# Kernel tuning notes

Hardware: AMD Instinct MI355X
Metric: run time of the kernel (lower is better)

## Reference

```python
import jax, jax.numpy as jnp
import numpy as np

B, T, D, H, L, P = 256, 96, 64, 256, 5, 14
H2 = 2 * H   # decoder hidden
O = D        # output_size must equal input_size (decoder feeds its own output back)


def setup_inputs() -> dict:
    key = jax.random.key(0)
    ks = iter(jax.random.split(key, 32))
    s = 0.08  # weight scale to keep gates out of saturation
    rn = lambda shape, sc=s: jax.random.normal(next(ks), shape, jnp.float32) * sc
    return dict(
        x=rn((B, T, D), 1.0),
        # encoder: bidirectional, layer 0 input=D, layers 1..4 input=2H
        enc_Wih0=rn((2, 4 * H, D)), enc_Whh0=rn((2, 4 * H, H)),
        enc_bih0=rn((2, 4 * H)), enc_bhh0=rn((2, 4 * H)),
        enc_Wih=rn((L - 1, 2, 4 * H, 2 * H)), enc_Whh=rn((L - 1, 2, 4 * H, H)),
        enc_bih=rn((L - 1, 2, 4 * H)), enc_bhh=rn((L - 1, 2, 4 * H)),
        # decoder: unidirectional, hidden=2H, layer 0 input=D, layers 1..4 input=2H
        dec_Wih0=rn((4 * H2, D)), dec_Whh0=rn((4 * H2, H2)),
        dec_bih0=rn((4 * H2,)), dec_bhh0=rn((4 * H2,)),
        dec_Wih=rn((L - 1, 4 * H2, H2)), dec_Whh=rn((L - 1, 4 * H2, H2)),
        dec_bih=rn((L - 1, 4 * H2)), dec_bhh=rn((L - 1, 4 * H2)),
        fc_W=rn((O, H2)), fc_b=rn((O,)),
    )


def _lstm_cell(x, h, c, Wih, Whh, bih, bhh):
    # PyTorch gate order: i, f, g, o
    g = x @ Wih.T + h @ Whh.T + (bih + bhh)
    i, f, gg, o = jnp.split(g, 4, axis=-1)
    c = jax.nn.sigmoid(f) * c + jax.nn.sigmoid(i) * jnp.tanh(gg)
    h = jax.nn.sigmoid(o) * jnp.tanh(c)
    return h, c


def _scan_dir(xs, Wih, Whh, bih, bhh, reverse):
    # xs: (T, B, Din); returns per-step hidden (T,B,Hn) + final (h, c)
    Bn, Hn = xs.shape[1], Whh.shape[-1]
    z = jnp.zeros((Bn, Hn), xs.dtype)

    def step(carry, xt):
        h, c = carry
        h, c = _lstm_cell(xt, h, c, Wih, Whh, bih, bhh)
        return (h, c), h

    (hT, cT), hs = jax.lax.scan(step, (z, z), xs, reverse=reverse)
    return hs, hT, cT


def _forward(x, enc_Wih0, enc_Whh0, enc_bih0, enc_bhh0,
             enc_Wih, enc_Whh, enc_bih, enc_bhh,
             dec_Wih0, dec_Whh0, dec_bih0, dec_bhh0,
             dec_Wih, dec_Whh, dec_bih, dec_bhh, fc_W, fc_b):
    xs = jnp.swapaxes(x, 0, 1)  # (T, B, D)
    inp = xs
    h_fin, c_fin = [], []
    for l in range(L):
        if l == 0:
            Wih, Whh, bih, bhh = enc_Wih0, enc_Whh0, enc_bih0, enc_bhh0
        else:
            Wih, Whh, bih, bhh = enc_Wih[l - 1], enc_Whh[l - 1], enc_bih[l - 1], enc_bhh[l - 1]
        hs_f, hTf, cTf = _scan_dir(inp, Wih[0], Whh[0], bih[0], bhh[0], False)
        hs_b, hTb, cTb = _scan_dir(inp, Wih[1], Whh[1], bih[1], bhh[1], True)
        inp = jnp.concatenate([hs_f, hs_b], axis=-1)  # (T, B, 2H)
        # matches h_n.view(L,2,B,H).transpose(1,2).view(L,B,2H): per layer [fwd, bwd]
        h_fin.append(jnp.concatenate([hTf, hTb], axis=-1))
        c_fin.append(jnp.concatenate([cTf, cTb], axis=-1))
    h0 = jnp.stack(h_fin)  # (L, B, 2H)
    c0 = jnp.stack(c_fin)

    dec_params = [(dec_Wih0, dec_Whh0, dec_bih0, dec_bhh0)] + \
                 [(dec_Wih[l], dec_Whh[l], dec_bih[l], dec_bhh[l]) for l in range(L - 1)]

    def dec_step(carry, _):
        h, c, xt = carry
        z = xt
        nh, nc = [], []
        for l, (Wih, Whh, bih, bhh) in enumerate(dec_params):
            hl, cl = _lstm_cell(z, h[l], c[l], Wih, Whh, bih, bhh)
            z = hl
            nh.append(hl); nc.append(cl)
        out = z @ fc_W.T + fc_b  # (B, O); fed back as next decoder input
        return (jnp.stack(nh), jnp.stack(nc), out), out

    _, outs = jax.lax.scan(dec_step, (h0, c0, x[:, -1, :]), None, length=P)
    return jnp.swapaxes(outs, 0, 1)  # (B, P, O)


def reference(x, enc_Wih0, enc_Whh0, enc_bih0, enc_bhh0,
              enc_Wih, enc_Whh, enc_bih, enc_bhh,
              dec_Wih0, dec_Whh0, dec_bih0, dec_bhh0,
              dec_Wih, dec_Whh, dec_bih, dec_bhh, fc_W, fc_b):
    return _forward(x, enc_Wih0, enc_Whh0, enc_bih0, enc_bhh0,
                    enc_Wih, enc_Whh, enc_bih, enc_bhh,
                    dec_Wih0, dec_Whh0, dec_bih0, dec_bhh0,
                    dec_Wih, dec_Whh, dec_bih, dec_bhh, fc_W, fc_b)
```

## Files before the change

### kernel.cpp

```cpp
#include <hip/hip_runtime.h>

typedef _Float16 f16;
using half8 = __attribute__((ext_vector_type(8))) _Float16;
using half4 = __attribute__((ext_vector_type(4))) _Float16;
using f32x4 = __attribute__((ext_vector_type(4))) float;

#define DEV __device__ __forceinline__
#define LD8(p) (*(const half8*)(const void*)(p))

DEV f32x4 mfma16(half8 a, half8 b, f32x4 c) {
  return __builtin_amdgcn_mfma_f32_16x16x32_f16(a, b, c, 0, 0, 0);
}
DEV float sigf(float x) { return 1.f / (1.f + __expf(-x)); }
DEV float tanhf2(float x) { float e = __expf(2.f * x); return 1.f - 2.f / (e + 1.f); }

static const size_t OFF_WIH0   = 0;
static const size_t OFF_WIH14  = 262144;
static const size_t OFF_WHH    = 8650752;
static const size_t OFF_WDEC0  = 13893632;
static const size_t OFF_WDEC14 = 16252928;
static const size_t OFF_WFC    = 33030144;
static const size_t OFF_X16    = 33095680;
static const size_t OFF_SEQA   = 36241408;
static const size_t OFF_SEQB   = 61407232;
static const size_t OFF_XG     = 86573056;
static const size_t OFF_HBUF   = 187236352;
static const size_t OFF_FLAGS  = 187760640;
static const size_t OFF_DHDB   = 188284928;
static const size_t OFF_DCST   = 190906368;
static const size_t OFF_ZFC    = 193527808;

__global__ __launch_bounds__(256) void prep(
    const float* __restrict__ x,
    const float* __restrict__ eWih0, const float* __restrict__ eWhh0,
    const float* __restrict__ eWih,  const float* __restrict__ eWhh,
    const float* __restrict__ dWih0, const float* __restrict__ dWhh0,
    const float* __restrict__ dWih,  const float* __restrict__ dWhh,
    const float* __restrict__ fcW,   char* __restrict__ ws)
{
  f16* wih0   = (f16*)(ws + OFF_WIH0);
  f16* wih14  = (f16*)(ws + OFF_WIH14);
  f16* whhf   = (f16*)(ws + OFF_WHH);
  f16* wdec0  = (f16*)(ws + OFF_WDEC0);
  f16* wdec14 = (f16*)(ws + OFF_WDEC14);
  f16* wfc    = (f16*)(ws + OFF_WFC);
  f16* x16    = (f16*)(ws + OFF_X16);
  f16* zfc    = (f16*)(ws + OFF_ZFC);
  int* flags  = (int*)(ws + OFF_FLAGS);
  const size_t total = 18137152;
  for (size_t i = (size_t)blockIdx.x * blockDim.x + threadIdx.x; i < total;
       i += (size_t)gridDim.x * blockDim.x) {
    size_t j = i;
    if (j < 131072) { wih0[j] = (f16)eWih0[j]; continue; }
    j -= 131072;
    if (j < 4194304) { wih14[j] = (f16)eWih[j]; continue; }
    j -= 4194304;
    if (j < 2621440) {
      size_t l = j >> 19, i2 = j & 524287;
      int d   = (int)(i2 >> 18);
      int uh  = (int)((i2 >> 17) & 1);
      int w   = (int)((i2 >> 14) & 7);
      int g   = (int)((i2 >> 12) & 3);
      int kc  = (int)((i2 >> 9) & 7);
      int lnv = (int)((i2 >> 3) & 63);
      int e   = (int)(i2 & 7);
      int unit = uh * 128 + w * 16 + (lnv & 15);
      int k = kc * 32 + (lnv >> 4) * 8 + e;
      int row = g * 256 + unit;
      float v = (l == 0) ? eWhh0[((size_t)d * 1024 + row) * 256 + k]
                         : eWhh[((((l - 1) * 2 + (size_t)d) * 1024) + row) * 256 + k];
      whhf[j] = (f16)v;
      continue;
    }
    j -= 2621440;
    if (j < 1179648) {
      size_t r = j / 576, c = j % 576;
      wdec0[j] = (f16)((c < 64) ? dWih0[r * 64 + c] : dWhh0[r * 512 + (c - 64)]);
      continue;
    }
    j -= 1179648;
    if (j < 8388608) {
      size_t l = j >> 21, rem = j & 2097151;
      size_t r = rem >> 10, c = rem & 1023;
      wdec14[j] = (f16)((c < 512) ? dWih[(l * 2048 + r) * 512 + c]
                                  : dWhh[(l * 2048 + r) * 512 + (c - 512)]);
      continue;
    }
    j -= 8388608;
    if (j < 32768) { wfc[j] = (f16)fcW[j]; continue; }
    j -= 32768;
    if (j < 1572864) {
      size_t t = j >> 14, rem = j & 16383;
      size_t b = rem >> 6, d = rem & 63;
      x16[j] = (f16)x[(b * 96 + t) * 64 + d];
      continue;
    }
    j -= 1572864;
    if (j < 16384) {
      size_t b = j >> 6, d = j & 63;
      zfc[b * 512 + d] = (f16)x[(b * 96 + 95) * 64 + d];
      continue;
    }
    j -= 16384;
    flags[j] = 0;
  }
}

__global__ __launch_bounds__(256) void gemm_xg(
    const f16* __restrict__ A, int K, const f16* __restrict__ W,
    const float* __restrict__ bih, const float* __restrict__ bhh,
    f16* __restrict__ xg)
{
  __shared__ __align__(16) f16 As[128 * 32];
  __shared__ __align__(16) f16 Ws[128 * 32];
  const int dir = blockIdx.y >> 3;
  const int cb  = (blockIdx.y & 7) * 128;
  const int rb  = blockIdx.x * 128;
  const int tid = threadIdx.x;
  const int wv = tid >> 6, ln = tid & 63;
  const int wr = wv >> 1, wc = wv & 1;
  const f16* Wd = W + (size_t)dir * 1024 * K;

  f32x4 acc[4][4];
#pragma unroll
  for (int m = 0; m < 4; m++)
#pragma unroll
    for (int n = 0; n < 4; n++) acc[m][n] = (f32x4){0.f, 0.f, 0.f, 0.f};

  const int sr = tid >> 1;
  const int sk = (tid & 1) * 16;
  const int nk = K >> 5;
  for (int kt = 0; kt < nk; ++kt) {
    half8 va0 = LD8(&A[(size_t)(rb + sr) * K + kt * 32 + sk]);
    half8 va1 = LD8(&A[(size_t)(rb + sr) * K + kt * 32 + sk + 8]);
    half8 vw0 = LD8(&Wd[(size_t)(cb + sr) * K + kt * 32 + sk]);
    half8 vw1 = LD8(&Wd[(size_t)(cb + sr) * K + kt * 32 + sk + 8]);
    *(half8*)&As[sr * 32 + sk] = va0;
    *(half8*)&As[sr * 32 + sk + 8] = va1;
    *(half8*)&Ws[sr * 32 + sk] = vw0;
    *(half8*)&Ws[sr * 32 + sk + 8] = vw1;
    __syncthreads();
    half8 af[4], bf[4];
#pragma unroll
    for (int m = 0; m < 4; m++)
      af[m] = LD8(&As[(wr * 64 + m * 16 + (ln & 15)) * 32 + (ln >> 4) * 8]);
#pragma unroll
    for (int n = 0; n < 4; n++)
      bf[n] = LD8(&Ws[(wc * 64 + n * 16 + (ln & 15)) * 32 + (ln >> 4) * 8]);
#pragma unroll
    for (int m = 0; m < 4; m++)
#pragma unroll
      for (int n = 0; n < 4; n++) acc[m][n] = mfma16(af[m], bf[n], acc[m][n]);
    __syncthreads();
  }
#pragma unroll
  for (int n = 0; n < 4; n++) {
    const int col = cb + wc * 64 + n * 16 + (ln & 15);
    const float bsum = bih[dir * 1024 + col] + bhh[dir * 1024 + col];
    const int c16 = (cb + wc * 64 + n * 16) >> 4;
#pragma unroll
    for (int m = 0; m < 4; m++) {
      const int r16 = (rb + wr * 64 + m * 16) >> 4;
      half4 h;
#pragma unroll
      for (int r = 0; r < 4; r++) h[r] = (f16)(acc[m][n][r] + bsum);
      *(half4*)&xg[(((size_t)dir * 1536 + r16) * 64 + c16) * 256 + ln * 4] = h;
    }
  }
}

__global__ __launch_bounds__(512) __attribute__((amdgpu_waves_per_eu(2, 2)))
void enc_layer(
    const f16* __restrict__ xg, const f16* __restrict__ whhf,
    f16* __restrict__ hbuf, int* __restrict__ flags,
    f16* __restrict__ seqo, f16* __restrict__ hfin, float* __restrict__ cfin,
    int layer)
{
  const int bb = blockIdx.x;
  const int d = blockIdx.y >> 1, uh = blockIdx.y & 1;
  const int tid = threadIdx.x;
  const int wv = tid >> 6, ln = tid & 63;
  const int lc = ln & 15, lk = ln >> 4;

  __shared__ __align__(16) char hl[2][4096];

  half8 wfr[32];
  const f16* wbase = whhf + (((size_t)(d * 2 + uh) * 8 + wv) * 16384);
#pragma unroll
  for (int g = 0; g < 4; g++) {
#pragma unroll
    for (int jj = 0; jj < 4; jj++) {
      wfr[g * 8 + jj]     = LD8(&wbase[(size_t)(g * 8 + uh * 4 + jj) * 512 + ln * 8]);
      wfr[g * 8 + 4 + jj] = LD8(&wbase[(size_t)(g * 8 + (1 - uh) * 4 + jj) * 512 + ln * 8]);
    }
  }
#pragma unroll
  for (int i = 0; i < 32; i++) asm volatile("" : "+v"(wfr[i]));

  f16* hown = hbuf + ((size_t)((bb * 2 + d) * 2 + uh)) * 4096;
  const f16* hpart = hbuf + ((size_t)((bb * 2 + d) * 2 + (uh ^ 1))) * 4096;
  int* myflag = &flags[(bb * 2 + d) * 2 + uh];
  int* pflag  = &flags[(bb * 2 + d) * 2 + (uh ^ 1)];
  const int base = layer * 96;
  const int rowbase = bb * 16;
  const int unit_local = wv * 16 + lc;
  const int cu = uh * 128 + unit_local;
  const int erow = tid >> 5, ec8 = tid & 31;
  const int eba = (erow * 256 + ec8 * 8) ^ ((erow & 7) << 4);

  f32x4 cst = (f32x4){0.f, 0.f, 0.f, 0.f};
  f32x4 ownp[4];
#pragma unroll
  for (int g = 0; g < 4; g++) ownp[g] = (f32x4){0.f, 0.f, 0.f, 0.f};

  for (int t = 0; t < 96; ++t) {
    const int tt = d ? 95 - t : t;
    const int par = (t - 1) & 1, par2 = t & 1;
    const int r16 = tt * 16 + bb;
    half4 xv[4];
#pragma unroll
    for (int g = 0; g < 4; g++)
      xv[g] = *(const half4*)&xg[(((size_t)d * 1536 + r16) * 64 +
                                  (g * 16 + uh * 8 + wv)) * 256 + ln * 4];
    f32x4 acc[4];
#pragma unroll
    for (int g = 0; g < 4; g++) {
#pragma unroll
      for (int r = 0; r < 4; r++) acc[g][r] = ownp[g][r] + (float)xv[g][r];
    }
    if (t > 0) {
      unsigned spin = 0;
      while (__hip_atomic_load(pflag, __ATOMIC_RELAXED,
                               __HIP_MEMORY_SCOPE_AGENT) < base + t) {
        if (++spin > 65536u) break;
      }
      asm volatile("" ::: "memory");
      unsigned long long q[4][2];
#pragma unroll
      for (int j = 0; j < 4; j++) {
        const f16* p = &hpart[par * 2048 + lc * 128 + j * 32 + lk * 8];
        q[j][0] = __hip_atomic_load((const unsigned long long*)p,
                                    __ATOMIC_RELAXED, __HIP_MEMORY_SCOPE_AGENT);
        q[j][1] = __hip_atomic_load((const unsigned long long*)(p + 4),
                                    __ATOMIC_RELAXED, __HIP_MEMORY_SCOPE_AGENT);
      }
#pragma unroll
      for (int j = 0; j < 4; j++) {
        union { unsigned long long uq[2]; half8 h; } u;
        u.uq[0] = q[j][0]; u.uq[1] = q[j][1];
#pragma unroll
        for (int g = 0; g < 4; g++)
          acc[g] = mfma16(u.h, wfr[g * 8 + 4 + j], acc[g]);
      }
    }
    f16 hv[4];
#pragma unroll
    for (int r = 0; r < 4; r++) {
      float gi = sigf(acc[0][r]);
      float gf = sigf(acc[1][r]);
      float gg = tanhf2(acc[2][r]);
      float go = sigf(acc[3][r]);
      float cn = gf * cst[r] + gi * gg;
      cst[r] = cn;
      hv[r] = (f16)(go * tanhf2(cn));
    }
#pragma unroll
    for (int r = 0; r < 4; r++) {
      int row = lk * 4 + r;
      int ba = (row * 256 + unit_local * 2) ^ ((row & 7) << 4);
      *(f16*)&hl[par2][ba] = hv[r];
    }
    __syncthreads();
    unsigned long long v = *(const unsigned long long*)&hl[par2][eba];
    __hip_atomic_store((unsigned long long*)&hown[par2 * 2048 + erow * 128 + ec8 * 4],
                       v, __ATOMIC_RELAXED, __HIP_MEMORY_SCOPE_AGENT);
    asm volatile("s_waitcnt vmcnt(0)" ::: "memory");
    __syncthreads();
    if (tid == 0)
      __hip_atomic_store(myflag, base + t + 1, __ATOMIC_RELAXED,
                         __HIP_MEMORY_SCOPE_AGENT);
    *(unsigned long long*)&seqo[(size_t)tt * 131072 +
        (size_t)(rowbase + erow) * 512 + d * 256 + uh * 128 + ec8 * 4] = v;
    if (t == 95) {
      *(unsigned long long*)&hfin[(size_t)(rowbase + erow) * 512 +
                                  d * 256 + uh * 128 + ec8 * 4] = v;
#pragma unroll
      for (int r = 0; r < 4; r++)
        cfin[(size_t)(rowbase + lk * 4 + r) * 512 + d * 256 + cu] = cst[r];
    } else {
      half8 ao[4];
#pragma unroll
      for (int j = 0; j < 4; j++) {
        int ba = (lc * 256 + j * 64 + lk * 16) ^ ((lc & 7) << 4);
        ao[j] = *(const half8*)&hl[par2][ba];
      }
#pragma unroll
      for (int g = 0; g < 4; g++) {
        f32x4 s = (f32x4){0.f, 0.f, 0.f, 0.f};
#pragma unroll
        for (int j = 0; j < 4; j++) s = mfma16(ao[j], wfr[g * 8 + j], s);
        ownp[g] = s;
      }
    }
  }
}

__global__ __launch_bounds__(128) void dec_step(
    const f16* __restrict__ A0, int K0, const f16* __restrict__ A1,
    const f16* __restrict__ W, int Kt,
    const float* __restrict__ bih, const float* __restrict__ bhh,
    float* __restrict__ cst, f16* __restrict__ h1)
{
  const int u0 = blockIdx.y * 32;
  const int rb = blockIdx.x * 64;
  const int wv = threadIdx.x >> 6, ln = threadIdx.x & 63;
  const int lc = ln & 15, lk = ln >> 4;
  const int cu = u0 + wv * 16 + lc;
  f32x4 acc[4][4];
#pragma unroll
  for (int g = 0; g < 4; g++) {
    float b = bih[g * 512 + cu] + bhh[g * 512 + cu];
#pragma unroll
    for (int rr = 0; rr < 4; rr++) acc[rr][g] = (f32x4){b, b, b, b};
  }
  const int K0c = K0 >> 5, Ktc = Kt >> 5;
  for (int kc = 0; kc < Ktc; kc++) {
    const f16* Ap; int ko;
    if (kc < K0c) { Ap = A0; ko = kc * 32; }
    else          { Ap = A1; ko = (kc - K0c) * 32; }
    half8 b[4];
#pragma unroll
    for (int g = 0; g < 4; g++)
      b[g] = LD8(&W[(size_t)(g * 512 + cu) * Kt + kc * 32 + lk * 8]);
#pragma unroll
    for (int rr = 0; rr < 4; rr++) {
      half8 a = LD8(&Ap[(size_t)(rb + rr * 16 + lc) * 512 + ko + lk * 8]);
#pragma unroll
      for (int g = 0; g < 4; g++) acc[rr][g] = mfma16(a, b[g], acc[rr][g]);
    }
  }
#pragma unroll
  for (int rr = 0; rr < 4; rr++) {
#pragma unroll
    for (int r = 0; r < 4; r++) {
      const int row = rb + rr * 16 + lk * 4 + r;
      float gi = sigf(acc[rr][0][r]);
      float gf = sigf(acc[rr][1][r]);
      float gg = tanhf2(acc[rr][2][r]);
      float go = sigf(acc[rr][3][r]);
      float cp = cst[(size_t)row * 512 + cu];
      float cn = gf * cp + gi * gg;
      cst[(size_t)row * 512 + cu] = cn;
      h1[(size_t)row * 512 + cu] = (f16)(go * tanhf2(cn));
    }
  }
}

__global__ __launch_bounds__(64) void fc_kernel(
    const f16* __restrict__ hin, const f16* __restrict__ Wf,
    const float* __restrict__ bf, float* __restrict__ out,
    f16* __restrict__ zfc, int s)
{
  const int rb = blockIdx.x * 16;
  const int ln = threadIdx.x;
  f32x4 acc[4];
#pragma unroll
  for (int n = 0; n < 4; n++) acc[n] = (f32x4){0.f, 0.f, 0.f, 0.f};
#pragma unroll
  for (int kc = 0; kc < 16; kc++) {
    half8 a = LD8(&hin[(size_t)(rb + (ln & 15)) * 512 + kc * 32 + (ln >> 4) * 8]);
#pragma unroll
    for (int n = 0; n < 4; n++) {
      half8 b = LD8(&Wf[(size_t)(n * 16 + (ln & 15)) * 512 + kc * 32 + (ln >> 4) * 8]);
      acc[n] = mfma16(a, b, acc[n]);
    }
  }
#pragma unroll
  for (int n = 0; n < 4; n++) {
    const int col = n * 16 + (ln & 15);
    const float bb = bf[col];
#pragma unroll
    for (int r = 0; r < 4; r++) {
      const int row = rb + (ln >> 4) * 4 + r;
      float v = acc[n][r] + bb;
      out[(size_t)row * 896 + s * 64 + col] = v;
      zfc[(size_t)row * 512 + col] = (f16)v;
    }
  }
}

extern "C" void kernel_launch(void* const* d_in, const int* in_sizes, int n_in,
                              void* d_out, int out_size, void* d_ws, size_t ws_size,
                              hipStream_t stream) {
  char* ws = (char*)d_ws;
  const float* x     = (const float*)d_in[0];
  const float* eWih0 = (const float*)d_in[1];
  const float* eWhh0 = (const float*)d_in[2];
  const float* ebih0 = (const float*)d_in[3];
  const float* ebhh0 = (const float*)d_in[4];
  const float* eWih  = (const float*)d_in[5];
  const float* eWhh  = (const float*)d_in[6];
  const float* ebih  = (const float*)d_in[7];
  const float* ebhh  = (const float*)d_in[8];
  const float* dWih0 = (const float*)d_in[9];
  const float* dWhh0 = (const float*)d_in[10];
  const float* dbih0 = (const float*)d_in[11];
  const float* dbhh0 = (const float*)d_in[12];
  const float* dWih  = (const float*)d_in[13];
  const float* dWhh  = (const float*)d_in[14];
  const float* dbih  = (const float*)d_in[15];
  const float* dbhh  = (const float*)d_in[16];
  const float* fcW   = (const float*)d_in[17];
  const float* fcb   = (const float*)d_in[18];

  f16* xg    = (f16*)(ws + OFF_XG);
  f16* hbuf  = (f16*)(ws + OFF_HBUF);
  int* flags = (int*)(ws + OFF_FLAGS);
  f16* dhdb  = (f16*)(ws + OFF_DHDB);
  float* dcst = (float*)(ws + OFF_DCST);
  f16* zfc   = (f16*)(ws + OFF_ZFC);
  f16* seqA  = (f16*)(ws + OFF_SEQA);
  f16* seqB  = (f16*)(ws + OFF_SEQB);

  prep<<<dim3(2048), dim3(256), 0, stream>>>(x, eWih0, eWhh0, eWih, eWhh,
                                             dWih0, dWhh0, dWih, dWhh, fcW, ws);

  for (int l = 0; l < 5; ++l) {
    const f16* Ain = (l == 0) ? (f16*)(ws + OFF_X16) : ((l & 1) ? seqA : seqB);
    const int K = (l == 0) ? 64 : 512;
    const f16* Wih = (l == 0) ? (f16*)(ws + OFF_WIH0)
                              : (f16*)(ws + OFF_WIH14) + (size_t)(l - 1) * 2 * 1024 * 512;
    const float* bi = (l == 0) ? ebih0 : ebih + (size_t)(l - 1) * 2048;
    const float* bh = (l == 0) ? ebhh0 : ebhh + (size_t)(l - 1) * 2048;
    gemm_xg<<<dim3(192, 16), dim3(256), 0, stream>>>(Ain, K, Wih, bi, bh, xg);

    const f16* whhf_l = (f16*)(ws + OFF_WHH) + (size_t)l * 524288;
    f16* so = (l & 1) ? seqB : seqA;
    enc_layer<<<dim3(16, 4), dim3(512), 0, stream>>>(
        xg, whhf_l, hbuf, flags, so,
        dhdb + (size_t)l * 131072, dcst + (size_t)l * 131072, l);
  }

  for (int s = 0; s < 14; ++s) {
    const int p = s & 1;
    for (int l = 0; l < 5; ++l) {
      dec_step<<<dim3(4, 16), dim3(128), 0, stream>>>(
          (l == 0) ? zfc : dhdb + (size_t)(p ^ 1) * 655360 + (size_t)(l - 1) * 131072,
          (l == 0) ? 64 : 512,
          dhdb + (size_t)p * 655360 + (size_t)l * 131072,
          (l == 0) ? (f16*)(ws + OFF_WDEC0)
                   : (f16*)(ws + OFF_WDEC14) + (size_t)(l - 1) * 2048 * 1024,
          (l == 0) ? 576 : 1024,
          (l == 0) ? dbih0 : dbih + (size_t)(l - 1) * 2048,
          (l == 0) ? dbhh0 : dbhh + (size_t)(l - 1) * 2048,
          dcst + (size_t)l * 131072,
          dhdb + (size_t)(p ^ 1) * 655360 + (size_t)l * 131072);
    }
    fc_kernel<<<dim3(16), dim3(64), 0, stream>>>(
        dhdb + (size_t)(p ^ 1) * 655360 + 4 * 131072, (f16*)(ws + OFF_WFC), fcb,
        (float*)d_out, zfc, s);
  }
}
```

Measured before the change: 4.279 ms.

## Split encoder recurrence across 8 unit-slices per direction with LDS-resident weights

Reworks the encoder recurrent kernel so each (batch block, direction) is served by 8 small 128-thread workgroups, each owning 32 hidden units, instead of 2 large 512-thread workgroups. Recurrent weights now sit in LDS rather than registers. Each step waits on flags from all 8 peers and reads the full hidden state from global memory, dropping the own-half precomputation trick. The aim is more parallel workgroups and less register pressure, at the cost of more cross-workgroup synchronisation and global traffic per timestep. The prep kernel's weight permutation and element count change to match the new layout.

```diff
diff --git a/kernel.cpp b/kernel.cpp
--- a/kernel.cpp
+++ b/kernel.cpp
@@ -47,7 +47,7 @@
   f16* x16    = (f16*)(ws + OFF_X16);
   f16* zfc    = (f16*)(ws + OFF_ZFC);
   int* flags  = (int*)(ws + OFF_FLAGS);
-  const size_t total = 18137152;
+  const size_t total = 18137344;
   for (size_t i = (size_t)blockIdx.x * blockDim.x + threadIdx.x; i < total;
        i += (size_t)gridDim.x * blockDim.x) {
     size_t j = i;
@@ -58,13 +58,13 @@
     if (j < 2621440) {
       size_t l = j >> 19, i2 = j & 524287;
       int d   = (int)(i2 >> 18);
-      int uh  = (int)((i2 >> 17) & 1);
-      int w   = (int)((i2 >> 14) & 7);
+      int uo  = (int)((i2 >> 15) & 7);
+      int tile= (int)((i2 >> 14) & 1);
       int g   = (int)((i2 >> 12) & 3);
       int kc  = (int)((i2 >> 9) & 7);
       int lnv = (int)((i2 >> 3) & 63);
       int e   = (int)(i2 & 7);
-      int unit = uh * 128 + w * 16 + (lnv & 15);
+      int unit = uo * 32 + tile * 16 + (lnv & 15);
       int k = kc * 32 + (lnv >> 4) * 8 + e;
       int row = g * 256 + unit;
       float v = (l == 0) ? eWhh0[((size_t)d * 1024 + row) * 256 + k]
@@ -169,49 +169,37 @@
   }
 }
 
-__global__ __launch_bounds__(512) __attribute__((amdgpu_waves_per_eu(2, 2)))
-void enc_layer(
+__global__ __launch_bounds__(128) void enc_layer(
     const f16* __restrict__ xg, const f16* __restrict__ whhf,
     f16* __restrict__ hbuf, int* __restrict__ flags,
     f16* __restrict__ seqo, f16* __restrict__ hfin, float* __restrict__ cfin,
     int layer)
 {
   const int bb = blockIdx.x;
-  const int d = blockIdx.y >> 1, uh = blockIdx.y & 1;
+  const int d = blockIdx.y >> 3, uo = blockIdx.y & 7;
   const int tid = threadIdx.x;
   const int wv = tid >> 6, ln = tid & 63;
   const int lc = ln & 15, lk = ln >> 4;
 
-  __shared__ __align__(16) char hl[2][4096];
-
-  half8 wfr[32];
-  const f16* wbase = whhf + (((size_t)(d * 2 + uh) * 8 + wv) * 16384);
-#pragma unroll
-  for (int g = 0; g < 4; g++) {
-#pragma unroll
-    for (int jj = 0; jj < 4; jj++) {
-      wfr[g * 8 + jj]     = LD8(&wbase[(size_t)(g * 8 + uh * 4 + jj) * 512 + ln * 8]);
-      wfr[g * 8 + 4 + jj] = LD8(&wbase[(size_t)(g * 8 + (1 - uh) * 4 + jj) * 512 + ln * 8]);
-    }
-  }
-#pragma unroll
-  for (int i = 0; i < 32; i++) asm volatile("" : "+v"(wfr[i]));
-
-  f16* hown = hbuf + ((size_t)((bb * 2 + d) * 2 + uh)) * 4096;
-  const f16* hpart = hbuf + ((size_t)((bb * 2 + d) * 2 + (uh ^ 1))) * 4096;
-  int* myflag = &flags[(bb * 2 + d) * 2 + uh];
-  int* pflag  = &flags[(bb * 2 + d) * 2 + (uh ^ 1)];
+  __shared__ __align__(16) f16 wL[32768];
+  __shared__ __align__(16) f16 hB[16 * 36];
+
+  const f16* wsrc = whhf + (size_t)(d * 8 + uo) * 32768;
+#pragma unroll 4
+  for (int i = 0; i < 32; i++)
+    *(half8*)&wL[(i * 128 + tid) * 8] = LD8(&wsrc[(size_t)(i * 128 + tid) * 8]);
+  __syncthreads();
+
+  int* gflags = &flags[(bb * 2 + d) * 8];
+  int* myflag = &gflags[uo];
+  const f16* hgrp = hbuf + (size_t)(bb * 2 + d) * 8192;
+  f16* hown = hbuf + (size_t)((bb * 2 + d) * 8 + uo) * 1024;
   const int base = layer * 96;
   const int rowbase = bb * 16;
-  const int unit_local = wv * 16 + lc;
-  const int cu = uh * 128 + unit_local;
-  const int erow = tid >> 5, ec8 = tid & 31;
-  const int eba = (erow * 256 + ec8 * 8) ^ ((erow & 7) << 4);
+  const int cu = uo * 32 + wv * 16 + lc;
+  const int erow = tid >> 3, eu8 = tid & 7;
 
   f32x4 cst = (f32x4){0.f, 0.f, 0.f, 0.f};
-  f32x4 ownp[4];
-#pragma unroll
-  for (int g = 0; g < 4; g++) ownp[g] = (f32x4){0.f, 0.f, 0.f, 0.f};
 
   for (int t = 0; t < 96; ++t) {
     const int tt = d ? 95 - t : t;
@@ -221,36 +209,48 @@
 #pragma unroll
     for (int g = 0; g < 4; g++)
       xv[g] = *(const half4*)&xg[(((size_t)d * 1536 + r16) * 64 +
-                                  (g * 16 + uh * 8 + wv)) * 256 + ln * 4];
-    f32x4 acc[4];
-#pragma unroll
-    for (int g = 0; g < 4; g++) {
-#pragma unroll
-      for (int r = 0; r < 4; r++) acc[g][r] = ownp[g][r] + (float)xv[g][r];
-    }
+                                  (g * 16 + uo * 2 + wv)) * 256 + ln * 4];
+    unsigned long long q[8][2];
     if (t > 0) {
-      unsigned spin = 0;
-      while (__hip_atomic_load(pflag, __ATOMIC_RELAXED,
-                               __HIP_MEMORY_SCOPE_AGENT) < base + t) {
-        if (++spin > 65536u) break;
+      if (tid == 0) {
+        unsigned spin = 0;
+        for (;;) {
+          int mn = 0x7fffffff;
+#pragma unroll
+          for (int p = 0; p < 8; p++) {
+            int f = __hip_atomic_load(&gflags[p], __ATOMIC_RELAXED,
+                                      __HIP_MEMORY_SCOPE_AGENT);
+            mn = (f < mn) ? f : mn;
+          }
+          if (mn >= base + t || ++spin > 100000u) break;
+          __builtin_amdgcn_s_sleep(1);
+        }
       }
-      asm volatile("" ::: "memory");
-      unsigned long long q[4][2];
-#pragma unroll
-      for (int j = 0; j < 4; j++) {
-        const f16* p = &hpart[par * 2048 + lc * 128 + j * 32 + lk * 8];
+      __syncthreads();
+#pragma unroll
+      for (int j = 0; j < 8; j++) {
+        const f16* p = hgrp + (size_t)(j * 2 + par) * 512 + lc * 32 + lk * 8;
         q[j][0] = __hip_atomic_load((const unsigned long long*)p,
                                     __ATOMIC_RELAXED, __HIP_MEMORY_SCOPE_AGENT);
         q[j][1] = __hip_atomic_load((const unsigned long long*)(p + 4),
                                     __ATOMIC_RELAXED, __HIP_MEMORY_SCOPE_AGENT);
       }
-#pragma unroll
-      for (int j = 0; j < 4; j++) {
+    }
+    f32x4 acc[4];
+#pragma unroll
+    for (int g = 0; g < 4; g++)
+      acc[g] = (f32x4){(float)xv[g][0], (float)xv[g][1],
+                       (float)xv[g][2], (float)xv[g][3]};
+    if (t > 0) {
+#pragma unroll
+      for (int j = 0; j < 8; j++) {
         union { unsigned long long uq[2]; half8 h; } u;
         u.uq[0] = q[j][0]; u.uq[1] = q[j][1];
 #pragma unroll
-        for (int g = 0; g < 4; g++)
-          acc[g] = mfma16(u.h, wfr[g * 8 + 4 + j], acc[g]);
+        for (int g = 0; g < 4; g++) {
+          half8 b = *(const half8*)&wL[(size_t)(((wv * 4 + g) * 8 + j) * 64 + ln) * 8];
+          acc[g] = mfma16(u.h, b, acc[g]);
+        }
       }
     }
     f16 hv[4];
@@ -265,14 +265,11 @@
       hv[r] = (f16)(go * tanhf2(cn));
     }
 #pragma unroll
-    for (int r = 0; r < 4; r++) {
-      int row = lk * 4 + r;
-      int ba = (row * 256 + unit_local * 2) ^ ((row & 7) << 4);
-      *(f16*)&hl[par2][ba] = hv[r];
-    }
+    for (int r = 0; r < 4; r++)
+      hB[(lk * 4 + r) * 36 + wv * 16 + lc] = hv[r];
     __syncthreads();
-    unsigned long long v = *(const unsigned long long*)&hl[par2][eba];
-    __hip_atomic_store((unsigned long long*)&hown[par2 * 2048 + erow * 128 + ec8 * 4],
+    unsigned long long v = *(const unsigned long long*)&hB[erow * 36 + eu8 * 4];
+    __hip_atomic_store((unsigned long long*)&hown[par2 * 512 + erow * 32 + eu8 * 4],
                        v, __ATOMIC_RELAXED, __HIP_MEMORY_SCOPE_AGENT);
     asm volatile("s_waitcnt vmcnt(0)" ::: "memory");
     __syncthreads();
@@ -280,27 +277,13 @@
       __hip_atomic_store(myflag, base + t + 1, __ATOMIC_RELAXED,
                          __HIP_MEMORY_SCOPE_AGENT);
     *(unsigned long long*)&seqo[(size_t)tt * 131072 +
-        (size_t)(rowbase + erow) * 512 + d * 256 + uh * 128 + ec8 * 4] = v;
+        (size_t)(rowbase + erow) * 512 + d * 256 + uo * 32 + eu8 * 4] = v;
     if (t == 95) {
       *(unsigned long long*)&hfin[(size_t)(rowbase + erow) * 512 +
-                                  d * 256 + uh * 128 + ec8 * 4] = v;
+                                  d * 256 + uo * 32 + eu8 * 4] = v;
 #pragma unroll
       for (int r = 0; r < 4; r++)
         cfin[(size_t)(rowbase + lk * 4 + r) * 512 + d * 256 + cu] = cst[r];
-    } else {
-      half8 ao[4];
-#pragma unroll
-      for (int j = 0; j < 4; j++) {
-        int ba = (lc * 256 + j * 64 + lk * 16) ^ ((lc & 7) << 4);
-        ao[j] = *(const half8*)&hl[par2][ba];
-      }
-#pragma unroll
-      for (int g = 0; g < 4; g++) {
-        f32x4 s = (f32x4){0.f, 0.f, 0.f, 0.f};
-#pragma unroll
-        for (int j = 0; j < 4; j++) s = mfma16(ao[j], wfr[g * 8 + j], s);
-        ownp[g] = s;
-      }
     }
   }
 }
@@ -436,7 +419,7 @@
 
     const f16* whhf_l = (f16*)(ws + OFF_WHH) + (size_t)l * 524288;
     f16* so = (l & 1) ? seqB : seqA;
-    enc_layer<<<dim3(16, 4), dim3(512), 0, stream>>>(
+    enc_layer<<<dim3(16, 16), dim3(128), 0, stream>>>(
         xg, whhf_l, hbuf, flags, so,
         dhdb + (size_t)l * 131072, dcst + (size_t)l * 131072, l);
   }
```

Result: faster. 3.863 ms (-9.7%).
